# Kernel tuning notes

Hardware: AMD Instinct MI355X
Metric: run time of the kernel (lower is better)

The kernel has to match this reference:

```python
import jax, jax.numpy as jnp
import numpy as np

BIG = 1e10
RADIUS = 0.5
NSAMPLE = 1


def square_distance(src, dst):
    # src: [B,N,3], dst: [B,M,3] -> [B,N,M] squared euclidean distances
    d = -2.0 * jnp.einsum('bnc,bmc->bnm', src, dst)
    d = d + jnp.sum(src ** 2, -1)[:, :, None]
    d = d + jnp.sum(dst ** 2, -1)[:, None, :]
    return d


def farthest_point_sample(xyz, npoint):
    # xyz: [B,N,3]; returns int32 indices [B,npoint]
    B, N, _ = xyz.shape
    dist0 = jnp.full((B, N), BIG, dtype=xyz.dtype)
    far0 = jnp.argmax(xyz[:, :, 0], axis=1).astype(jnp.int32)

    def step(carry, _):
        dist, far = carry
        centroid = jnp.take_along_axis(xyz, far[:, None, None], axis=1)  # [B,1,3]
        d = jnp.sum((xyz - centroid) ** 2, -1)  # [B,N]
        dist = jnp.minimum(dist, d)
        new_far = jnp.argmax(dist, axis=-1).astype(jnp.int32)
        return (dist, new_far), far  # record PRE-update farthest, like the torch loop

    (_, _), centroids = jax.lax.scan(step, (dist0, far0), None, length=npoint)
    return centroids.T  # [B,npoint]


def index_points(points, idx):
    # points: [B,N,C], idx: [B,S] -> [B,S,C]
    return jnp.take_along_axis(points, idx[:, :, None], axis=1)


def query_ball_point(radius, nsample, xyz, new_xyz):
    # xyz: [B,N,3], new_xyz: [B,S,3] -> int32 [B,S,nsample]
    B, S, _ = new_xyz.shape
    N = xyz.shape[1]
    sqrdists = square_distance(new_xyz, xyz)  # [B,S,N]
    base = jnp.arange(N, dtype=jnp.int32)
    group_idx = jnp.where(sqrdists > radius ** 2, jnp.int32(N), base)  # [B,S,N]
    group_idx = jnp.sort(group_idx, axis=-1)[:, :, :nsample]
    group_first = jnp.broadcast_to(group_idx[:, :, :1], group_idx.shape)
    group_idx = jnp.where(group_idx == N, group_first, group_idx)
    return group_idx


def setup_inputs() -> dict:
    key = jax.random.key(0)
    k1, k2 = jax.random.split(key)
    B, N = 4, 16384
    xyz = jax.random.uniform(k1, (B, 3, N), dtype=jnp.float32)
    cls_label = jax.random.uniform(k2, (B, 16), dtype=jnp.float32)
    return {"xyz": xyz, "cls_label": cls_label, "npoint": 1024}


def reference(xyz, cls_label, npoint):
    pts = jnp.transpose(xyz, (0, 2, 1))  # [B,N,3]
    centroids = farthest_point_sample(pts, npoint)  # [B,S]
    new_xyz = index_points(pts, centroids)  # [B,S,3]
    idx = query_ball_point(RADIUS, NSAMPLE, pts, new_xyz)  # [B,S,1]
    return idx
```

## Files before the change

### kernel.cpp

```cpp
#include <hip/hip_runtime.h>


constexpr int N_PTS  = 16384;
constexpr int NPOINT = 1024;
constexpr int BLOCK  = 512;
constexpr int KPT    = N_PTS / BLOCK;
constexpr int NWAVE  = BLOCK / 64;

__device__ inline unsigned long long pack_key(float v, int idx) {
    return ((unsigned long long)__float_as_uint(v) << 32) |
           (unsigned)(N_PTS - 1 - idx);
}
__device__ inline int key_idx(unsigned long long k) {
    return N_PTS - 1 - (int)(k & 0xFFFFu);
}

__global__ __launch_bounds__(BLOCK, 2) void fps_kernel(
    const float* __restrict__ xyz,
    int* __restrict__ cent)
{
    const int b   = blockIdx.x;
    const int tid = threadIdx.x;
    const float* X = xyz + (size_t)b * 3 * N_PTS;
    const float* Y = X + N_PTS;
    const float* Z = X + 2 * N_PTS;

    float px[KPT], py[KPT], pz[KPT], dst[KPT];
#pragma unroll
    for (int k = 0; k < KPT; ++k) {
        const int p = tid + k * BLOCK;
        px[k] = X[p];
        py[k] = Y[p];
        pz[k] = Z[p];
        dst[k] = 1e10f;
    }

    __shared__ unsigned long long s_key[2][NWAVE];

    const int wave = tid >> 6;
    const int lane = tid & 63;

    {
        float bv = px[0];
        int   bi = tid;
#pragma unroll
        for (int k = 1; k < KPT; ++k) {
            if (px[k] > bv) { bv = px[k]; bi = tid + k * BLOCK; }
        }
        unsigned long long key = pack_key(bv, bi);
#pragma unroll
        for (int off = 32; off > 0; off >>= 1) {
            unsigned long long o = __shfl_xor(key, off);
            if (o > key) key = o;
        }
        if (lane == 0) s_key[0][wave] = key;
    }
    __syncthreads();
    unsigned long long bk = s_key[0][0];
#pragma unroll
    for (int w = 1; w < NWAVE; ++w) {
        const unsigned long long o = s_key[0][w];
        if (o > bk) bk = o;
    }
    int far = __builtin_amdgcn_readfirstlane(key_idx(bk));

    for (int it = 0; it < NPOINT; ++it) {
        if (tid == 0) cent[b * NPOINT + it] = far;
        if (it == NPOINT - 1) break;

        const float cx = X[far];
        const float cy = Y[far];
        const float cz = Z[far];

        float nbv = -1.0f;
        int   nbi = N_PTS;
#pragma unroll
        for (int k = 0; k < KPT; ++k) {
            const float dx = __fsub_rn(px[k], cx);
            const float dy = __fsub_rn(py[k], cy);
            const float dz = __fsub_rn(pz[k], cz);
            const float d  = __fadd_rn(
                __fadd_rn(__fmul_rn(dx, dx), __fmul_rn(dy, dy)),
                __fmul_rn(dz, dz));
            const float nd = fminf(dst[k], d);
            dst[k] = nd;
            if (nd > nbv) { nbv = nd; nbi = tid + k * BLOCK; }
        }

        unsigned long long key = pack_key(nbv, nbi);
#pragma unroll
        for (int off = 32; off > 0; off >>= 1) {
            unsigned long long o = __shfl_xor(key, off);
            if (o > key) key = o;
        }
        const int buf = (it + 1) & 1;
        if (lane == 0) s_key[buf][wave] = key;
        __syncthreads();

        unsigned long long k0 = s_key[buf][0];
#pragma unroll
        for (int w = 1; w < NWAVE; ++w) {
            const unsigned long long o = s_key[buf][w];
            if (o > k0) k0 = o;
        }
        far = __builtin_amdgcn_readfirstlane(key_idx(k0));
    }
}

__global__ __launch_bounds__(256) void ballq_kernel(
    const float* __restrict__ xyz,
    const int* __restrict__ cent,
    int* __restrict__ out)
{
    const int gw   = (blockIdx.x * 256 + threadIdx.x) >> 6;
    const int lane = threadIdx.x & 63;
    const int b = gw / NPOINT;
    const int s = gw % NPOINT;

    const float* X = xyz + (size_t)b * 3 * N_PTS;
    const float* Y = X + N_PTS;
    const float* Z = X + 2 * N_PTS;

    const int ci = cent[b * NPOINT + s];
    const float cx = X[ci];
    const float cy = Y[ci];
    const float cz = Z[ci];
    const float cn = __fadd_rn(
        __fadd_rn(__fmul_rn(cx, cx), __fmul_rn(cy, cy)), __fmul_rn(cz, cz));

    int res = N_PTS;
    for (int base = 0; base < N_PTS; base += 64) {
        const int p = base + lane;
        const float x = X[p];
        const float y = Y[p];
        const float z = Z[p];
        const float dot = __fadd_rn(
            __fadd_rn(__fmul_rn(x, cx), __fmul_rn(y, cy)), __fmul_rn(z, cz));
        const float pn = __fadd_rn(
            __fadd_rn(__fmul_rn(x, x), __fmul_rn(y, y)), __fmul_rn(z, z));
        const float d = __fadd_rn(__fadd_rn(__fmul_rn(-2.0f, dot), cn), pn);
        const bool hit = !(d > 0.25f);
        const unsigned long long m = __ballot(hit);
        if (m) {
            res = base + (__ffsll((long long)m) - 1);
            break;
        }
    }
    if (lane == 0) out[b * NPOINT + s] = res;
}

extern "C" void kernel_launch(void* const* d_in, const int* in_sizes, int n_in,
                              void* d_out, int out_size, void* d_ws, size_t ws_size,
                              hipStream_t stream) {
    const float* xyz = (const float*)d_in[0];
    const int B = in_sizes[1] / 16;
    int* cent = (int*)d_ws;
    int* out  = (int*)d_out;

    fps_kernel<<<B, BLOCK, 0, stream>>>(xyz, cent);

    const int nwaves  = B * NPOINT;
    const int nblocks = nwaves / 4;
    ballq_kernel<<<nblocks, 256, 0, stream>>>(xyz, cent, out);
}
```

Baseline: 1.869 ms.

## Split FPS per batch across 8 cooperating blocks with global atomic barrier

Farthest point sampling now splits each batch's points across 8 workgroups instead of one. Each iteration does a block-local reduction, then a global atomic max on a per-iteration key slot and an atomic counter, spinning until all 8 blocks have arrived. This spreads the serial per-iteration distance update over more compute units, at the cost of a device-scope atomic and spin barrier every iteration. It also relies on all 32 blocks being co-resident, and it adds a memset of the workspace. The original single-block path is kept as a fallback when the workspace is too small.

```diff
diff --git a/kernel.cpp b/kernel.cpp
--- a/kernel.cpp
+++ b/kernel.cpp
@@ -1,11 +1,15 @@
 #include <hip/hip_runtime.h>
 
 
-constexpr int N_PTS  = 16384;
-constexpr int NPOINT = 1024;
-constexpr int BLOCK  = 512;
-constexpr int KPT    = N_PTS / BLOCK;
-constexpr int NWAVE  = BLOCK / 64;
+constexpr int   N_PTS  = 16384;
+constexpr int   NPOINT = 1024;
+constexpr float BIGF   = 1e10f;
+
+constexpr int T     = 512;
+constexpr int G     = 8;
+constexpr int CHUNK = N_PTS / G;
+constexpr int KPT   = CHUNK / T;
+constexpr int NWAVE = T / 64;
 
 __device__ inline unsigned long long pack_key(float v, int idx) {
     return ((unsigned long long)__float_as_uint(v) << 32) |
@@ -15,57 +19,79 @@
     return N_PTS - 1 - (int)(k & 0xFFFFu);
 }
 
-__global__ __launch_bounds__(BLOCK, 2) void fps_kernel(
+__global__ __launch_bounds__(T, 2) void fps_multi(
     const float* __restrict__ xyz,
+    unsigned long long* __restrict__ keyArr,
+    unsigned int* __restrict__ cnt,
     int* __restrict__ cent)
 {
-    const int b   = blockIdx.x;
-    const int tid = threadIdx.x;
+    const int b    = blockIdx.x / G;
+    const int g    = blockIdx.x % G;
+    const int tid  = threadIdx.x;
+    const int wave = tid >> 6;
+    const int lane = tid & 63;
+
     const float* X = xyz + (size_t)b * 3 * N_PTS;
     const float* Y = X + N_PTS;
     const float* Z = X + 2 * N_PTS;
+    const int base = g * CHUNK;
 
     float px[KPT], py[KPT], pz[KPT], dst[KPT];
 #pragma unroll
     for (int k = 0; k < KPT; ++k) {
-        const int p = tid + k * BLOCK;
-        px[k] = X[p];
-        py[k] = Y[p];
-        pz[k] = Z[p];
-        dst[k] = 1e10f;
+        const int p = base + k * T + tid;
+        px[k]  = X[p];
+        py[k]  = Y[p];
+        pz[k]  = Z[p];
+        dst[k] = BIGF;
     }
 
     __shared__ unsigned long long s_key[2][NWAVE];
-
-    const int wave = tid >> 6;
-    const int lane = tid & 63;
-
-    {
-        float bv = px[0];
-        int   bi = tid;
-#pragma unroll
-        for (int k = 1; k < KPT; ++k) {
-            if (px[k] > bv) { bv = px[k]; bi = tid + k * BLOCK; }
-        }
-        unsigned long long key = pack_key(bv, bi);
+    unsigned long long* krow = keyArr + (size_t)b * NPOINT;
+    unsigned int*       crow = cnt    + (size_t)b * NPOINT;
+
+    auto sync_reduce = [&](unsigned long long key, int r) -> int {
 #pragma unroll
         for (int off = 32; off > 0; off >>= 1) {
-            unsigned long long o = __shfl_xor(key, off);
+            const unsigned long long o = __shfl_xor(key, off);
             if (o > key) key = o;
         }
-        if (lane == 0) s_key[0][wave] = key;
-    }
-    __syncthreads();
-    unsigned long long bk = s_key[0][0];
-#pragma unroll
-    for (int w = 1; w < NWAVE; ++w) {
-        const unsigned long long o = s_key[0][w];
-        if (o > bk) bk = o;
-    }
-    int far = __builtin_amdgcn_readfirstlane(key_idx(bk));
+        const int buf = r & 1;
+        if (lane == 0) s_key[buf][wave] = key;
+        __syncthreads();
+        unsigned long long bk = s_key[buf][0];
+#pragma unroll
+        for (int w = 1; w < NWAVE; ++w) {
+            const unsigned long long o = s_key[buf][w];
+            if (o > bk) bk = o;
+        }
+        if (tid == 0) {
+            __hip_atomic_fetch_max(&krow[r], bk, __ATOMIC_RELAXED,
+                                   __HIP_MEMORY_SCOPE_AGENT);
+            __hip_atomic_fetch_add(&crow[r], 1u, __ATOMIC_RELEASE,
+                                   __HIP_MEMORY_SCOPE_AGENT);
+        }
+        unsigned int c;
+        do {
+            c = __hip_atomic_load(&crow[r], __ATOMIC_ACQUIRE,
+                                  __HIP_MEMORY_SCOPE_AGENT);
+        } while (c < (unsigned)G);
+        const unsigned long long gk =
+            __hip_atomic_load(&krow[r], __ATOMIC_RELAXED,
+                              __HIP_MEMORY_SCOPE_AGENT);
+        return __builtin_amdgcn_readfirstlane(key_idx(gk));
+    };
+
+    float bv = px[0];
+    int   bi = base + tid;
+#pragma unroll
+    for (int k = 1; k < KPT; ++k) {
+        if (px[k] > bv) { bv = px[k]; bi = base + k * T + tid; }
+    }
+    int far = sync_reduce(pack_key(bv, bi), 0);
 
     for (int it = 0; it < NPOINT; ++it) {
-        if (tid == 0) cent[b * NPOINT + it] = far;
+        if (g == 0 && tid == 0) cent[(size_t)b * NPOINT + it] = far;
         if (it == NPOINT - 1) break;
 
         const float cx = X[far];
@@ -73,7 +99,7 @@
         const float cz = Z[far];
 
         float nbv = -1.0f;
-        int   nbi = N_PTS;
+        int   nbi = 0;
 #pragma unroll
         for (int k = 0; k < KPT; ++k) {
             const float dx = __fsub_rn(px[k], cx);
@@ -84,26 +110,81 @@
                 __fmul_rn(dz, dz));
             const float nd = fminf(dst[k], d);
             dst[k] = nd;
-            if (nd > nbv) { nbv = nd; nbi = tid + k * BLOCK; }
-        }
-
-        unsigned long long key = pack_key(nbv, nbi);
+            if (nd > nbv) { nbv = nd; nbi = base + k * T + tid; }
+        }
+        far = sync_reduce(pack_key(nbv, nbi), it + 1);
+    }
+}
+
+__global__ __launch_bounds__(512, 2) void fps_single(
+    const float* __restrict__ xyz,
+    int* __restrict__ cent)
+{
+    constexpr int BL = 512, KP = N_PTS / BL, NW = BL / 64;
+    const int b   = blockIdx.x;
+    const int tid = threadIdx.x;
+    const float* X = xyz + (size_t)b * 3 * N_PTS;
+    const float* Y = X + N_PTS;
+    const float* Z = X + 2 * N_PTS;
+
+    float px[KP], py[KP], pz[KP], dst[KP];
+#pragma unroll
+    for (int k = 0; k < KP; ++k) {
+        const int p = tid + k * BL;
+        px[k] = X[p]; py[k] = Y[p]; pz[k] = Z[p]; dst[k] = BIGF;
+    }
+    __shared__ unsigned long long s_key[2][NW];
+    const int wave = tid >> 6, lane = tid & 63;
+
+    float bv = px[0]; int bi = tid;
+#pragma unroll
+    for (int k = 1; k < KP; ++k)
+        if (px[k] > bv) { bv = px[k]; bi = tid + k * BL; }
+    unsigned long long key = pack_key(bv, bi);
+#pragma unroll
+    for (int off = 32; off > 0; off >>= 1) {
+        const unsigned long long o = __shfl_xor(key, off);
+        if (o > key) key = o;
+    }
+    if (lane == 0) s_key[0][wave] = key;
+    __syncthreads();
+    unsigned long long bk = s_key[0][0];
+#pragma unroll
+    for (int w = 1; w < NW; ++w)
+        if (s_key[0][w] > bk) bk = s_key[0][w];
+    int far = __builtin_amdgcn_readfirstlane(key_idx(bk));
+
+    for (int it = 0; it < NPOINT; ++it) {
+        if (tid == 0) cent[b * NPOINT + it] = far;
+        if (it == NPOINT - 1) break;
+        const float cx = X[far], cy = Y[far], cz = Z[far];
+        float nbv = -1.0f; int nbi = 0;
+#pragma unroll
+        for (int k = 0; k < KP; ++k) {
+            const float dx = __fsub_rn(px[k], cx);
+            const float dy = __fsub_rn(py[k], cy);
+            const float dz = __fsub_rn(pz[k], cz);
+            const float d  = __fadd_rn(
+                __fadd_rn(__fmul_rn(dx, dx), __fmul_rn(dy, dy)),
+                __fmul_rn(dz, dz));
+            const float nd = fminf(dst[k], d);
+            dst[k] = nd;
+            if (nd > nbv) { nbv = nd; nbi = tid + k * BL; }
+        }
+        unsigned long long k2 = pack_key(nbv, nbi);
 #pragma unroll
         for (int off = 32; off > 0; off >>= 1) {
-            unsigned long long o = __shfl_xor(key, off);
-            if (o > key) key = o;
+            const unsigned long long o = __shfl_xor(k2, off);
+            if (o > k2) k2 = o;
         }
         const int buf = (it + 1) & 1;
-        if (lane == 0) s_key[buf][wave] = key;
+        if (lane == 0) s_key[buf][wave] = k2;
         __syncthreads();
-
-        unsigned long long k0 = s_key[buf][0];
-#pragma unroll
-        for (int w = 1; w < NWAVE; ++w) {
-            const unsigned long long o = s_key[buf][w];
-            if (o > k0) k0 = o;
-        }
-        far = __builtin_amdgcn_readfirstlane(key_idx(k0));
+        unsigned long long b2 = s_key[buf][0];
+#pragma unroll
+        for (int w = 1; w < NW; ++w)
+            if (s_key[buf][w] > b2) b2 = s_key[buf][w];
+        far = __builtin_amdgcn_readfirstlane(key_idx(b2));
     }
 }
 
@@ -122,25 +203,20 @@
     const float* Z = X + 2 * N_PTS;
 
     const int ci = cent[b * NPOINT + s];
-    const float cx = X[ci];
-    const float cy = Y[ci];
-    const float cz = Z[ci];
+    const float cx = X[ci], cy = Y[ci], cz = Z[ci];
     const float cn = __fadd_rn(
         __fadd_rn(__fmul_rn(cx, cx), __fmul_rn(cy, cy)), __fmul_rn(cz, cz));
 
     int res = N_PTS;
     for (int base = 0; base < N_PTS; base += 64) {
         const int p = base + lane;
-        const float x = X[p];
-        const float y = Y[p];
-        const float z = Z[p];
+        const float x = X[p], y = Y[p], z = Z[p];
         const float dot = __fadd_rn(
             __fadd_rn(__fmul_rn(x, cx), __fmul_rn(y, cy)), __fmul_rn(z, cz));
         const float pn = __fadd_rn(
             __fadd_rn(__fmul_rn(x, x), __fmul_rn(y, y)), __fmul_rn(z, z));
         const float d = __fadd_rn(__fadd_rn(__fmul_rn(-2.0f, dot), cn), pn);
-        const bool hit = !(d > 0.25f);
-        const unsigned long long m = __ballot(hit);
+        const unsigned long long m = __ballot(!(d > 0.25f));
         if (m) {
             res = base + (__ffsll((long long)m) - 1);
             break;
@@ -154,12 +230,22 @@
                               hipStream_t stream) {
     const float* xyz = (const float*)d_in[0];
     const int B = in_sizes[1] / 16;
-    int* cent = (int*)d_ws;
-    int* out  = (int*)d_out;
-
-    fps_kernel<<<B, BLOCK, 0, stream>>>(xyz, cent);
-
-    const int nwaves  = B * NPOINT;
-    const int nblocks = nwaves / 4;
-    ballq_kernel<<<nblocks, 256, 0, stream>>>(xyz, cent, out);
-}
+    int* out = (int*)d_out;
+
+    const size_t keyBytes  = (size_t)B * NPOINT * sizeof(unsigned long long);
+    const size_t cntBytes  = (size_t)B * NPOINT * sizeof(unsigned int);
+    const size_t centBytes = (size_t)B * NPOINT * sizeof(int);
+
+    if (ws_size >= keyBytes + cntBytes + centBytes) {
+        unsigned long long* keyArr = (unsigned long long*)d_ws;
+        unsigned int* cnt  = (unsigned int*)((char*)d_ws + keyBytes);
+        int*          cent = (int*)((char*)d_ws + keyBytes + cntBytes);
+        hipMemsetAsync(d_ws, 0, keyBytes + cntBytes, stream);
+        fps_multi<<<B * G, T, 0, stream>>>(xyz, keyArr, cnt, cent);
+        ballq_kernel<<<B * NPOINT / 4, 256, 0, stream>>>(xyz, cent, out);
+    } else {
+        int* cent = (int*)d_ws;
+        fps_single<<<B, 512, 0, stream>>>(xyz, cent);
+        ballq_kernel<<<B * NPOINT / 4, 256, 0, stream>>>(xyz, cent, out);
+    }
+}
```

Measured after the change: 7.467 ms. +299.4%, slower.

## Rework FPS kernel with 1024-thread blocks, packed float2 math and DPP argmax

Applied to the files above, without the earlier changes.

The FPS kernel now runs 1024 threads per block, and each thread owns a contiguous run of points loaded as float2 pairs so the distance update can use packed FP32 math. The 64-bit key shuffle reduction is replaced by a DPP-based float wave max, a ballot to pick the first matching lane, and a per-wave value/index exchange through shared memory. The aim is to shorten the serial per-iteration critical path: fewer points per thread and a cheaper cross-lane reduction. Tie-breaking on index may differ from the reference ordering because lanes now hold contiguous points. There is also a fallback that places centroids in the output buffer when the workspace is too small.

```diff
diff --git a/kernel.cpp b/kernel.cpp
--- a/kernel.cpp
+++ b/kernel.cpp
@@ -1,68 +1,90 @@
 #include <hip/hip_runtime.h>
 
 
-constexpr int N_PTS  = 16384;
-constexpr int NPOINT = 1024;
-constexpr int BLOCK  = 512;
-constexpr int KPT    = N_PTS / BLOCK;
-constexpr int NWAVE  = BLOCK / 64;
+constexpr int   N_PTS  = 16384;
+constexpr int   NPOINT = 1024;
+constexpr int   BLOCK  = 1024;
+constexpr int   KPT    = N_PTS / BLOCK;
+constexpr int   NPAIR  = KPT / 2;
+constexpr int   NWAVE  = BLOCK / 64;
+constexpr float BIGF   = 1e10f;
 
-__device__ inline unsigned long long pack_key(float v, int idx) {
-    return ((unsigned long long)__float_as_uint(v) << 32) |
-           (unsigned)(N_PTS - 1 - idx);
-}
-__device__ inline int key_idx(unsigned long long k) {
-    return N_PTS - 1 - (int)(k & 0xFFFFu);
+typedef float v2f __attribute__((ext_vector_type(2)));
+
+__device__ inline float wave_max_f32(float v) {
+    int x = __float_as_int(v);
+    int t;
+    t = __builtin_amdgcn_update_dpp(x, x, 0x111, 0xf, 0xf, false);
+    x = __float_as_int(fmaxf(__int_as_float(x), __int_as_float(t)));
+    t = __builtin_amdgcn_update_dpp(x, x, 0x112, 0xf, 0xf, false);
+    x = __float_as_int(fmaxf(__int_as_float(x), __int_as_float(t)));
+    t = __builtin_amdgcn_update_dpp(x, x, 0x114, 0xf, 0xf, false);
+    x = __float_as_int(fmaxf(__int_as_float(x), __int_as_float(t)));
+    t = __builtin_amdgcn_update_dpp(x, x, 0x118, 0xf, 0xf, false);
+    x = __float_as_int(fmaxf(__int_as_float(x), __int_as_float(t)));
+    t = __builtin_amdgcn_update_dpp(x, x, 0x142, 0xa, 0xf, false);
+    x = __float_as_int(fmaxf(__int_as_float(x), __int_as_float(t)));
+    t = __builtin_amdgcn_update_dpp(x, x, 0x143, 0xc, 0xf, false);
+    x = __float_as_int(fmaxf(__int_as_float(x), __int_as_float(t)));
+    return __int_as_float(__builtin_amdgcn_readlane(x, 63));
 }
 
-__global__ __launch_bounds__(BLOCK, 2) void fps_kernel(
+__global__ __launch_bounds__(BLOCK) void fps_kernel(
     const float* __restrict__ xyz,
     int* __restrict__ cent)
 {
-    const int b   = blockIdx.x;
-    const int tid = threadIdx.x;
+#pragma clang fp contract(off)
+    const int b    = blockIdx.x;
+    const int tid  = threadIdx.x;
+    const int wave = tid >> 6;
+    const int lane = tid & 63;
+    const int pb   = tid * KPT;
+
     const float* X = xyz + (size_t)b * 3 * N_PTS;
     const float* Y = X + N_PTS;
     const float* Z = X + 2 * N_PTS;
 
-    float px[KPT], py[KPT], pz[KPT], dst[KPT];
+    v2f px[NPAIR], py[NPAIR], pz[NPAIR], dst[NPAIR];
 #pragma unroll
-    for (int k = 0; k < KPT; ++k) {
-        const int p = tid + k * BLOCK;
-        px[k] = X[p];
-        py[k] = Y[p];
-        pz[k] = Z[p];
-        dst[k] = 1e10f;
+    for (int j = 0; j < NPAIR; ++j) {
+        px[j]  = *(const v2f*)(X + pb + 2 * j);
+        py[j]  = *(const v2f*)(Y + pb + 2 * j);
+        pz[j]  = *(const v2f*)(Z + pb + 2 * j);
+        dst[j] = (v2f){BIGF, BIGF};
     }
 
-    __shared__ unsigned long long s_key[2][NWAVE];
+    __shared__ uint2 s_red[2][NWAVE];
 
-    const int wave = tid >> 6;
-    const int lane = tid & 63;
+    auto block_argmax = [&](float val, int idx, int r) -> int {
+        const float mv = wave_max_f32(val);
+        const unsigned long long cand = __ballot(val == mv);
+        const int fl   = __ffsll((long long)cand) - 1;
+        const int widx = __builtin_amdgcn_readlane(idx, fl);
+        const int buf  = r & 1;
+        if (lane == 0) {
+            s_red[buf][wave] = make_uint2(__float_as_uint(mv), (unsigned)widx);
+        }
+        __syncthreads();
+        uint2 e0 = s_red[buf][0];
+        float bv = __uint_as_float(e0.x);
+        int   bi = (int)e0.y;
+#pragma unroll
+        for (int w = 1; w < NWAVE; ++w) {
+            const uint2 e = s_red[buf][w];
+            const float v = __uint_as_float(e.x);
+            if (v > bv) { bv = v; bi = (int)e.y; }
+        }
+        return __builtin_amdgcn_readfirstlane(bi);
+    };
 
-    {
-        float bv = px[0];
-        int   bi = tid;
+    float bv = -1.0f;
+    int   bi = 0;
 #pragma unroll
-        for (int k = 1; k < KPT; ++k) {
-            if (px[k] > bv) { bv = px[k]; bi = tid + k * BLOCK; }
-        }
-        unsigned long long key = pack_key(bv, bi);
-#pragma unroll
-        for (int off = 32; off > 0; off >>= 1) {
-            unsigned long long o = __shfl_xor(key, off);
-            if (o > key) key = o;
-        }
-        if (lane == 0) s_key[0][wave] = key;
+    for (int j = 0; j < NPAIR; ++j) {
+        if (px[j].x > bv) { bv = px[j].x; bi = pb + 2 * j; }
+        if (px[j].y > bv) { bv = px[j].y; bi = pb + 2 * j + 1; }
     }
-    __syncthreads();
-    unsigned long long bk = s_key[0][0];
-#pragma unroll
-    for (int w = 1; w < NWAVE; ++w) {
-        const unsigned long long o = s_key[0][w];
-        if (o > bk) bk = o;
-    }
-    int far = __builtin_amdgcn_readfirstlane(key_idx(bk));
+    int far = block_argmax(bv, bi, 0);
 
     for (int it = 0; it < NPOINT; ++it) {
         if (tid == 0) cent[b * NPOINT + it] = far;
@@ -71,39 +93,24 @@
         const float cx = X[far];
         const float cy = Y[far];
         const float cz = Z[far];
+        const v2f c2x = {cx, cx}, c2y = {cy, cy}, c2z = {cz, cz};
 
         float nbv = -1.0f;
-        int   nbi = N_PTS;
+        int   nbi = 0;
 #pragma unroll
-        for (int k = 0; k < KPT; ++k) {
-            const float dx = __fsub_rn(px[k], cx);
-            const float dy = __fsub_rn(py[k], cy);
-            const float dz = __fsub_rn(pz[k], cz);
-            const float d  = __fadd_rn(
-                __fadd_rn(__fmul_rn(dx, dx), __fmul_rn(dy, dy)),
-                __fmul_rn(dz, dz));
-            const float nd = fminf(dst[k], d);
-            dst[k] = nd;
-            if (nd > nbv) { nbv = nd; nbi = tid + k * BLOCK; }
+        for (int j = 0; j < NPAIR; ++j) {
+            const v2f dx = px[j] - c2x;
+            const v2f dy = py[j] - c2y;
+            const v2f dz = pz[j] - c2z;
+            const v2f d  = (dx * dx + dy * dy) + dz * dz;
+            v2f nd;
+            nd.x = fminf(dst[j].x, d.x);
+            nd.y = fminf(dst[j].y, d.y);
+            dst[j] = nd;
+            if (nd.x > nbv) { nbv = nd.x; nbi = pb + 2 * j; }
+            if (nd.y > nbv) { nbv = nd.y; nbi = pb + 2 * j + 1; }
         }
-
-        unsigned long long key = pack_key(nbv, nbi);
-#pragma unroll
-        for (int off = 32; off > 0; off >>= 1) {
-            unsigned long long o = __shfl_xor(key, off);
-            if (o > key) key = o;
-        }
-        const int buf = (it + 1) & 1;
-        if (lane == 0) s_key[buf][wave] = key;
-        __syncthreads();
-
-        unsigned long long k0 = s_key[buf][0];
-#pragma unroll
-        for (int w = 1; w < NWAVE; ++w) {
-            const unsigned long long o = s_key[buf][w];
-            if (o > k0) k0 = o;
-        }
-        far = __builtin_amdgcn_readfirstlane(key_idx(k0));
+        far = block_argmax(nbv, nbi, it + 1);
     }
 }
 
@@ -122,25 +129,20 @@
     const float* Z = X + 2 * N_PTS;
 
     const int ci = cent[b * NPOINT + s];
-    const float cx = X[ci];
-    const float cy = Y[ci];
-    const float cz = Z[ci];
+    const float cx = X[ci], cy = Y[ci], cz = Z[ci];
     const float cn = __fadd_rn(
         __fadd_rn(__fmul_rn(cx, cx), __fmul_rn(cy, cy)), __fmul_rn(cz, cz));
 
     int res = N_PTS;
     for (int base = 0; base < N_PTS; base += 64) {
         const int p = base + lane;
-        const float x = X[p];
-        const float y = Y[p];
-        const float z = Z[p];
+        const float x = X[p], y = Y[p], z = Z[p];
         const float dot = __fadd_rn(
             __fadd_rn(__fmul_rn(x, cx), __fmul_rn(y, cy)), __fmul_rn(z, cz));
         const float pn = __fadd_rn(
             __fadd_rn(__fmul_rn(x, x), __fmul_rn(y, y)), __fmul_rn(z, z));
         const float d = __fadd_rn(__fadd_rn(__fmul_rn(-2.0f, dot), cn), pn);
-        const bool hit = !(d > 0.25f);
-        const unsigned long long m = __ballot(hit);
+        const unsigned long long m = __ballot(!(d > 0.25f));
         if (m) {
             res = base + (__ffsll((long long)m) - 1);
             break;
@@ -154,12 +156,11 @@
                               hipStream_t stream) {
     const float* xyz = (const float*)d_in[0];
     const int B = in_sizes[1] / 16;
-    int* cent = (int*)d_ws;
-    int* out  = (int*)d_out;
+    int* out = (int*)d_out;
+
+    int* cent = (ws_size >= (size_t)B * NPOINT * sizeof(int)) ? (int*)d_ws
+                                                              : (int*)d_out;
 
     fps_kernel<<<B, BLOCK, 0, stream>>>(xyz, cent);
-
-    const int nwaves  = B * NPOINT;
-    const int nblocks = nwaves / 4;
-    ballq_kernel<<<nblocks, 256, 0, stream>>>(xyz, cent, out);
+    ballq_kernel<<<B * NPOINT / 4, 256, 0, stream>>>(xyz, cent, out);
 }
```

Result: slower. 2.140 ms (+14.5%).
